# Performance work log

Measured on AMD Instinct MI355X. Metric: run time of the kernel, lower is better.

Reference implementation:

```python
import jax, jax.numpy as jnp
import numpy as np

N = 50000      # num nodes
E = 400000     # num edges
B = 64         # num graphs
D_IN = 768
DIMS = [512, 256, 128]
CH = 64        # classifier hidden
NC = 2         # num classes
EPS = 1e-5


def setup_inputs() -> dict:
    key = jax.random.key(0)
    ks = jax.random.split(key, 12)
    inp = {}
    inp["x"] = jax.random.normal(ks[0], (N, D_IN), jnp.float32)
    inp["edge_index"] = jax.random.randint(ks[1], (2, E), 0, N, dtype=jnp.int32)
    inp["batch"] = jnp.sort(jax.random.randint(ks[2], (N,), 0, B, dtype=jnp.int32))
    dims = [D_IN] + DIMS
    for i in range(3):
        inp[f"W{i}"] = jax.random.normal(ks[3 + i], (dims[i], dims[i + 1]), jnp.float32) / np.sqrt(dims[i]).astype(np.float32)
        inp[f"b{i}"] = jnp.zeros((dims[i + 1],), jnp.float32)
        inp[f"gamma{i}"] = jnp.ones((dims[i + 1],), jnp.float32)
        inp[f"beta{i}"] = jnp.zeros((dims[i + 1],), jnp.float32)
    inp["Wc1"] = jax.random.normal(ks[6], (2 * DIMS[-1], CH), jnp.float32) / np.sqrt(2 * DIMS[-1]).astype(np.float32)
    inp["bc1"] = jnp.zeros((CH,), jnp.float32)
    inp["gamma_c"] = jnp.ones((CH,), jnp.float32)
    inp["beta_c"] = jnp.zeros((CH,), jnp.float32)
    inp["Wc2"] = jax.random.normal(ks[7], (CH, NC), jnp.float32) / np.sqrt(CH).astype(np.float32)
    inp["bc2"] = jnp.zeros((NC,), jnp.float32)
    return inp


def _batchnorm(h, gamma, beta):
    # training-mode BatchNorm1d: biased batch statistics over the node axis
    m = jnp.mean(h, axis=0)
    v = jnp.var(h, axis=0)
    return (h - m) * jax.lax.rsqrt(v + EPS) * gamma + beta


def _forward(x, edge_index, batch, params):
    # GCN normalization with self-loops: norm_e = deg[src]^-1/2 * deg[dst]^-1/2
    loops = jnp.arange(N, dtype=edge_index.dtype)
    src = jnp.concatenate([edge_index[0], loops])
    dst = jnp.concatenate([edge_index[1], loops])
    deg = jax.ops.segment_sum(jnp.ones_like(dst, jnp.float32), dst, num_segments=N)
    dis = jax.lax.rsqrt(deg)  # deg >= 1 due to self loops
    norm = dis[src] * dis[dst]  # [E+N]

    n_layers = len(params)
    h = x
    for i, (W, b, g, be) in enumerate(params):
        hw = h @ W                                   # [N, out_dim]
        msg = hw[src] * norm[:, None]                # gather + scale, [E+N, out_dim]
        h = jax.ops.segment_sum(msg, dst, num_segments=N) + b
        h = _batchnorm(h, g, be)
        if i < n_layers - 1:
            h = jax.nn.relu(h)
        # dropout: identity in eval; residual never fires (dims 512/256 != 128)
    return h


def reference(x, edge_index, batch,
              W0, b0, gamma0, beta0,
              W1, b1, gamma1, beta1,
              W2, b2, gamma2, beta2,
              Wc1, bc1, gamma_c, beta_c, Wc2, bc2):
    params = [(W0, b0, gamma0, beta0), (W1, b1, gamma1, beta1), (W2, b2, gamma2, beta2)]
    h = _forward(x, edge_index, batch, params)       # [N, 128]

    # mean_max global pooling over graphs
    ones = jnp.ones((N,), jnp.float32)
    cnt = jnp.maximum(jax.ops.segment_sum(ones, batch, num_segments=B), 1.0)
    mean_pool = jax.ops.segment_sum(h, batch, num_segments=B) / cnt[:, None]
    max_pool = jax.ops.segment_max(h, batch, num_segments=B)
    g = jnp.concatenate([mean_pool, max_pool], axis=1)  # [B, 256]

    # classifier: Linear -> ReLU -> BatchNorm -> (Dropout=id) -> Linear
    hc = jax.nn.relu(g @ Wc1 + bc1)
    hc = _batchnorm(hc, gamma_c, beta_c)
    logits = hc @ Wc2 + bc2                          # [B, 2]
    return logits
```

## Files before the change

### kernel.cpp

```cpp
#include <hip/hip_runtime.h>
#include <cstddef>

#define NN 50000
#define EE 400000
#define BB 64
#define MP 50048
#define BN_EPS 1e-5f
#define PSEG 32

typedef __attribute__((ext_vector_type(8))) short s16x8;
typedef __attribute__((ext_vector_type(4))) float f32x4;
typedef __attribute__((ext_vector_type(8))) _Float16 f16x8;

#define GLOAD_LDS16(g, l) __builtin_amdgcn_global_load_lds( \
    (const __attribute__((address_space(1))) void*)(g),     \
    (__attribute__((address_space(3))) void*)(l), 16, 0, 0)

__global__ void fill_f32(float* __restrict__ p, int n, float v) {
    int i = blockIdx.x * blockDim.x + threadIdx.x;
    if (i < n) p[i] = v;
}

__global__ void fill_i32(int* __restrict__ p, int n, int v) {
    int i = blockIdx.x * blockDim.x + threadIdx.x;
    if (i < n) p[i] = v;
}

__global__ void deg_edges(const int* __restrict__ ei, int* __restrict__ deg) {
    int e = blockIdx.x * blockDim.x + threadIdx.x;
    if (e < EE) atomicAdd(&deg[ei[EE + e]], 1);
}

__global__ void cvt_wt_planes(const float* __restrict__ W,
                              unsigned short* __restrict__ Wh,
                              unsigned short* __restrict__ Wl,
                              int K, int N) {
    int i = blockIdx.x * blockDim.x + threadIdx.x;
    if (i >= K * N) return;
    int k = i / N, n = i % N;
    float f = W[i];
    unsigned int fb = __float_as_uint(f);
    unsigned int hif = fb & 0xFFFF0000u;
    float lo = f - __uint_as_float(hif);
    Wh[(size_t)n * K + k] = (unsigned short)(hif >> 16);
    Wl[(size_t)n * K + k] = (unsigned short)(__float_as_uint(lo) >> 16);
}

__global__ __launch_bounds__(256) void scan_block(const int* __restrict__ deg,
                                                  int* __restrict__ rowptr,
                                                  int* __restrict__ bsum,
                                                  float* __restrict__ dis) {
    __shared__ int tmp[256];
    int tid = threadIdx.x;
    int i = blockIdx.x * 256 + tid;
    int v = (i < NN) ? deg[i] : 0;
    if (i < NN) dis[i] = rsqrtf((float)v + 1.0f);
    tmp[tid] = v;
    __syncthreads();
#pragma unroll
    for (int off = 1; off < 256; off <<= 1) {
        int t = (tid >= off) ? tmp[tid - off] : 0;
        __syncthreads();
        tmp[tid] += t;
        __syncthreads();
    }
    if (i < NN) rowptr[i] = tmp[tid] - v;
    if (tid == 255) bsum[blockIdx.x] = tmp[255];
}

__global__ __launch_bounds__(256) void scan_sums(const int* __restrict__ bsum,
                                                 int* __restrict__ boff, int nb) {
    __shared__ int tmp[256];
    int tid = threadIdx.x;
    int v = (tid < nb) ? bsum[tid] : 0;
    tmp[tid] = v;
    __syncthreads();
#pragma unroll
    for (int off = 1; off < 256; off <<= 1) {
        int t = (tid >= off) ? tmp[tid - off] : 0;
        __syncthreads();
        tmp[tid] += t;
        __syncthreads();
    }
    boff[tid] = tmp[tid] - v;
}

__global__ void scan_fixup(int* __restrict__ rowptr, const int* __restrict__ boff,
                           int* __restrict__ cursor) {
    int i = blockIdx.x * blockDim.x + threadIdx.x;
    if (i < NN) {
        int v = rowptr[i] + boff[i >> 8];
        rowptr[i] = v;
        cursor[i] = v;
    }
    if (i == 0) rowptr[NN] = EE;
}

__global__ void fill_csr(const int* __restrict__ ei, int* __restrict__ cursor,
                         int* __restrict__ csr_src) {
    int e = blockIdx.x * blockDim.x + threadIdx.x;
    if (e >= EE) return;
    int s = ei[e];
    int t = ei[EE + e];
    int pos = atomicAdd(&cursor[t], 1);
    csr_src[pos] = s;
}

static __device__ __forceinline__ void unpack_pk(const uint4& u0, const uint4& u1,
                                                 s16x8& h, s16x8& l) {
    unsigned int p[8] = {u0.x, u0.y, u0.z, u0.w, u1.x, u1.y, u1.z, u1.w};
    union { s16x8 v; unsigned int u[4]; } H, L;
#pragma unroll
    for (int k = 0; k < 4; ++k) {
        H.u[k] = (p[2 * k + 1] & 0xFFFF0000u) | (p[2 * k] >> 16);
        L.u[k] = (p[2 * k + 1] << 16) | (p[2 * k] & 0xFFFFu);
    }
    h = H.v; l = L.v;
}

static __device__ __forceinline__ void unpack_f32(const uint4& u0, const uint4& u1,
                                                  s16x8& h, s16x8& l) {
    unsigned int e[8] = {u0.x, u0.y, u0.z, u0.w, u1.x, u1.y, u1.z, u1.w};
    unsigned int hi[8], lo[8];
#pragma unroll
    for (int j = 0; j < 8; ++j) {
        hi[j] = e[j] & 0xFFFF0000u;
        float lf = __uint_as_float(e[j]) - __uint_as_float(hi[j]);
        lo[j] = __float_as_uint(lf);
    }
    union { s16x8 v; unsigned int u[4]; } H, L;
#pragma unroll
    for (int k = 0; k < 4; ++k) {
        H.u[k] = (hi[2 * k + 1]) | (hi[2 * k] >> 16);
        L.u[k] = (lo[2 * k + 1] & 0xFFFF0000u) | (lo[2 * k] >> 16);
    }
    h = H.v; l = L.v;
}

template <int AMODE>
__global__ __launch_bounds__(256) void gemm_split3(const unsigned int* __restrict__ A,
                                                   const unsigned short* __restrict__ Bh,
                                                   const unsigned short* __restrict__ Bl,
                                                   _Float16* __restrict__ C,
                                                   const float* __restrict__ dis,
                                                   int K, int N) {
    __shared__ unsigned int As[128 * 32];
    __shared__ unsigned short Bsh[128 * 32];
    __shared__ unsigned short Bsl[128 * 32];
    const int tid = threadIdx.x;
    const int w  = tid >> 6;
    const int lw = tid & 63;
    const int lo = lw & 15;
    const int hi = lw >> 4;
    const int wr = w >> 1, wc = w & 1;
    const int rowBase = blockIdx.y * 128;
    const int colBase = blockIdx.x * 128;

    const int arow = w * 8 + (lw >> 3);
    const int acol = (lw & 7) * 4;
    const int brow = w * 16 + (lw >> 2);
    const int bcol = (lw & 3) * 8;

    f32x4 acc[4][4];
#pragma unroll
    for (int m = 0; m < 4; ++m)
#pragma unroll
        for (int n = 0; n < 4; ++n) acc[m][n] = (f32x4){0.f, 0.f, 0.f, 0.f};

    for (int k0 = 0; k0 < K; k0 += 32) {
#pragma unroll
        for (int i = 0; i < 4; ++i) {
            int gr = rowBase + i * 32 + arow;
            gr = (gr < NN) ? gr : (NN - 1);
            GLOAD_LDS16(A + (size_t)gr * K + k0 + acol, (char*)As + i * 4096 + w * 1024);
        }
#pragma unroll
        for (int j = 0; j < 2; ++j) {
            int gc = colBase + j * 64 + brow;
            GLOAD_LDS16(Bh + (size_t)gc * K + k0 + bcol, (char*)Bsh + j * 4096 + w * 1024);
            GLOAD_LDS16(Bl + (size_t)gc * K + k0 + bcol, (char*)Bsl + j * 4096 + w * 1024);
        }
        __syncthreads();

        s16x8 ah[4], al[4], bh[4], bl[4];
#pragma unroll
        for (int m = 0; m < 4; ++m) {
            int r = wr * 64 + m * 16 + lo;
            uint4 u0 = *(const uint4*)&As[r * 32 + hi * 8];
            uint4 u1 = *(const uint4*)&As[r * 32 + hi * 8 + 4];
            if (AMODE == 0) unpack_f32(u0, u1, ah[m], al[m]);
            else            unpack_pk(u0, u1, ah[m], al[m]);
        }
#pragma unroll
        for (int n = 0; n < 4; ++n) {
            int r = wc * 64 + n * 16 + lo;
            bh[n] = *(const s16x8*)&Bsh[r * 32 + hi * 8];
            bl[n] = *(const s16x8*)&Bsl[r * 32 + hi * 8];
        }
#pragma unroll
        for (int m = 0; m < 4; ++m)
#pragma unroll
            for (int n = 0; n < 4; ++n) {
                acc[m][n] = __builtin_amdgcn_mfma_f32_16x16x32_bf16(ah[m], bh[n], acc[m][n], 0, 0, 0);
                acc[m][n] = __builtin_amdgcn_mfma_f32_16x16x32_bf16(ah[m], bl[n], acc[m][n], 0, 0, 0);
                acc[m][n] = __builtin_amdgcn_mfma_f32_16x16x32_bf16(al[m], bh[n], acc[m][n], 0, 0, 0);
            }
        __syncthreads();
    }

#pragma unroll
    for (int m = 0; m < 4; ++m) {
        int row0 = rowBase + wr * 64 + m * 16 + hi * 4;
#pragma unroll
        for (int j = 0; j < 4; ++j) {
            int r = row0 + j;
            float ds = dis[(r < NN) ? r : (NN - 1)];
#pragma unroll
            for (int n = 0; n < 4; ++n) {
                int col = colBase + wc * 64 + n * 16 + lo;
                C[(size_t)r * N + col] = (_Float16)(ds * acc[m][n][j]);
            }
        }
    }
}

__global__ __launch_bounds__(256) void agg_gather(const _Float16* __restrict__ hws,
                                                  float* __restrict__ agg,
                                                  const int* __restrict__ rowptr,
                                                  const int* __restrict__ csr_src,
                                                  const float* __restrict__ dis,
                                                  const float* __restrict__ bias,
                                                  int D) {
    const int tpn = D >> 3;
    const int npb = 256 / tpn;
    const int local = threadIdx.x / tpn;
    const int lane = threadIdx.x % tpn;
    const int n = blockIdx.x * npb + local;
    if (n >= NN) return;
    const int dq = lane * 8;

    f16x8 sv = *(const f16x8*)&hws[(size_t)n * D + dq];
    float a[8];
#pragma unroll
    for (int j = 0; j < 8; ++j) a[j] = (float)sv[j];

    int e0 = rowptr[n], e1 = rowptr[n + 1];
    int e = e0;
    for (; e + 4 <= e1; e += 4) {
        int s0 = csr_src[e + 0];
        int s1 = csr_src[e + 1];
        int s2 = csr_src[e + 2];
        int s3 = csr_src[e + 3];
        f16x8 v0 = *(const f16x8*)&hws[(size_t)s0 * D + dq];
        f16x8 v1 = *(const f16x8*)&hws[(size_t)s1 * D + dq];
        f16x8 v2 = *(const f16x8*)&hws[(size_t)s2 * D + dq];
        f16x8 v3 = *(const f16x8*)&hws[(size_t)s3 * D + dq];
#pragma unroll
        for (int j = 0; j < 8; ++j)
            a[j] += ((float)v0[j] + (float)v1[j]) + ((float)v2[j] + (float)v3[j]);
    }
    for (; e < e1; ++e) {
        int s = csr_src[e];
        f16x8 v = *(const f16x8*)&hws[(size_t)s * D + dq];
#pragma unroll
        for (int j = 0; j < 8; ++j) a[j] += (float)v[j];
    }

    float din = dis[n];
    f32x4 o0, o1;
#pragma unroll
    for (int j = 0; j < 4; ++j) o0[j] = din * a[j] + bias[dq + j];
#pragma unroll
    for (int j = 0; j < 4; ++j) o1[j] = din * a[4 + j] + bias[dq + 4 + j];
    *(f32x4*)&agg[(size_t)n * D + dq] = o0;
    *(f32x4*)&agg[(size_t)n * D + dq + 4] = o1;
}

__global__ void bn_stats(const float* __restrict__ h, float* __restrict__ stats, int D) {
    int d = blockIdx.x * blockDim.x + threadIdx.x;
    if (d >= D) return;
    float s = 0.f, ss = 0.f;
    for (int n = blockIdx.y; n < NN; n += gridDim.y) {
        float v = h[(size_t)n * D + d];
        s += v;
        ss += v * v;
    }
    atomicAdd(&stats[d], s);
    atomicAdd(&stats[D + d], ss);
}

__global__ void bn_apply(unsigned int* __restrict__ buf,
                         const float* __restrict__ stats,
                         const float* __restrict__ gamma, const float* __restrict__ beta,
                         int D) {
    size_t i = (size_t)blockIdx.x * blockDim.x + threadIdx.x;
    if (i >= (size_t)NN * D) return;
    int d = (int)(i % (size_t)D);
    float mean = stats[d] * (1.0f / NN);
    float var  = stats[D + d] * (1.0f / NN) - mean * mean;
    float f = (__uint_as_float(buf[i]) - mean) * rsqrtf(var + BN_EPS) * gamma[d] + beta[d];
    f = fmaxf(f, 0.f);
    unsigned int fb = __float_as_uint(f);
    unsigned int hif = fb & 0xFFFF0000u;
    float lf = f - __uint_as_float(hif);
    buf[i] = hif | (__float_as_uint(lf) >> 16);
}

__global__ void bn_coef(const float* __restrict__ stats,
                        const float* __restrict__ gamma, const float* __restrict__ beta,
                        float* __restrict__ c1, float* __restrict__ c2, int D) {
    int d = blockIdx.x * blockDim.x + threadIdx.x;
    if (d >= D) return;
    float mean = stats[d] * (1.0f / NN);
    float var  = stats[D + d] * (1.0f / NN) - mean * mean;
    float r = rsqrtf(var + BN_EPS) * gamma[d];
    c1[d] = r;
    c2[d] = beta[d] - mean * r;
}

__global__ void find_starts(const int* __restrict__ batch, int* __restrict__ start) {
    int n = blockIdx.x * blockDim.x + threadIdx.x;
    if (n >= NN) return;
    int bc = batch[n];
    int bp = (n == 0) ? -1 : batch[n - 1];
    for (int g = bp + 1; g <= bc; ++g) start[g] = n;
    if (n == NN - 1) {
        for (int g = bc + 1; g <= BB; ++g) start[g] = NN;
    }
}

__global__ void pool_part(const float* __restrict__ h, const int* __restrict__ start,
                          const float* __restrict__ c1, const float* __restrict__ c2,
                          float* __restrict__ part) {
    int b = blockIdx.x;
    int seg = blockIdx.y;
    int d = threadIdx.x;
    int s0 = start[b], s1 = start[b + 1];
    int len = s1 - s0;
    int a = s0 + (int)((long long)len * seg / PSEG);
    int e = s0 + (int)((long long)len * (seg + 1) / PSEG);
    float a1 = c1[d], a2 = c2[d];
    float sum = 0.f;
    float mx = -3.402823466e+38f;
    for (int n = a; n < e; ++n) {
        float v = a1 * h[(size_t)n * 128 + d] + a2;
        sum += v;
        mx = fmaxf(mx, v);
    }
    part[(size_t)(b * PSEG + seg) * 256 + d] = sum;
    part[(size_t)(b * PSEG + seg) * 256 + 128 + d] = mx;
}

__global__ void pool_reduce(const float* __restrict__ part, const int* __restrict__ start,
                            float* __restrict__ pool) {
    int b = blockIdx.x;
    int d = threadIdx.x;
    float sum = 0.f;
    float mx = -3.402823466e+38f;
    for (int s = 0; s < PSEG; ++s) {
        sum += part[(size_t)(b * PSEG + s) * 256 + d];
        mx = fmaxf(mx, part[(size_t)(b * PSEG + s) * 256 + 128 + d]);
    }
    float cnt = fmaxf((float)(start[b + 1] - start[b]), 1.0f);
    pool[b * 256 + d] = sum / cnt;
    pool[b * 256 + 128 + d] = mx;
}

__global__ __launch_bounds__(256) void classifier_kernel(
        const float* __restrict__ pool,
        const float* __restrict__ Wc1, const float* __restrict__ bc1,
        const float* __restrict__ gc, const float* __restrict__ bec,
        const float* __restrict__ Wc2, const float* __restrict__ bc2,
        float* __restrict__ out) {
    __shared__ float hc[64][65];
    __shared__ float cmean[64];
    __shared__ float crstd[64];
    int tid = threadIdx.x;

    for (int i = tid; i < 64 * 64; i += 256) {
        int r = i / 64, c = i % 64;
        float acc = bc1[c];
        for (int k = 0; k < 256; ++k)
            acc += pool[r * 256 + k] * Wc1[k * 64 + c];
        hc[r][c] = fmaxf(acc, 0.f);
    }
    __syncthreads();

    if (tid < 64) {
        float s = 0.f, ss = 0.f;
        for (int r = 0; r < 64; ++r) {
            float v = hc[r][tid];
            s += v;
            ss += v * v;
        }
        float m = s * (1.0f / 64.0f);
        float var = ss * (1.0f / 64.0f) - m * m;
        cmean[tid] = m;
        crstd[tid] = rsqrtf(var + BN_EPS);
    }
    __syncthreads();

    if (tid < 128) {
        int r = tid / 2, k = tid % 2;
        float acc = bc2[k];
        for (int c = 0; c < 64; ++c) {
            float v = (hc[r][c] - cmean[c]) * crstd[c] * gc[c] + bec[c];
            acc += v * Wc2[c * 2 + k];
        }
        out[r * 2 + k] = acc;
    }
}

extern "C" void kernel_launch(void* const* d_in, const int* in_sizes, int n_in,
                              void* d_out, int out_size, void* d_ws, size_t ws_size,
                              hipStream_t stream) {
    const float* x     = (const float*)d_in[0];
    const int*   ei    = (const int*)d_in[1];
    const int*   batch = (const int*)d_in[2];
    const float* W[3]  = {(const float*)d_in[3], (const float*)d_in[7], (const float*)d_in[11]};
    const float* bbv[3] = {(const float*)d_in[4], (const float*)d_in[8], (const float*)d_in[12]};
    const float* gm[3] = {(const float*)d_in[5], (const float*)d_in[9], (const float*)d_in[13]};
    const float* bt[3] = {(const float*)d_in[6], (const float*)d_in[10], (const float*)d_in[14]};
    const float* Wc1 = (const float*)d_in[15];
    const float* bc1 = (const float*)d_in[16];
    const float* gc  = (const float*)d_in[17];
    const float* bec = (const float*)d_in[18];
    const float* Wc2 = (const float*)d_in[19];
    const float* bc2 = (const float*)d_in[20];
    float* out = (float*)d_out;

    char* p = (char*)d_ws;
    _Float16* hw = (_Float16*)p; p += (size_t)MP * 512 * 2;
    unsigned int* agg = (unsigned int*)p; p += (size_t)NN * 512 * 4;
    unsigned short* Wh[3];
    unsigned short* Wl[3];
    Wh[0] = (unsigned short*)p; p += (size_t)512 * 768 * 2;
    Wl[0] = (unsigned short*)p; p += (size_t)512 * 768 * 2;
    Wh[1] = (unsigned short*)p; p += (size_t)256 * 512 * 2;
    Wl[1] = (unsigned short*)p; p += (size_t)256 * 512 * 2;
    Wh[2] = (unsigned short*)p; p += (size_t)128 * 256 * 2;
    Wl[2] = (unsigned short*)p; p += (size_t)128 * 256 * 2;
    float* dis   = (float*)p; p += (size_t)NN * 4;
    float* stats = (float*)p; p += 1024 * 4;
    float* pool  = (float*)p; p += (size_t)BB * 256 * 4;
    float* part  = (float*)p; p += (size_t)BB * PSEG * 256 * 4;
    int* deg_i   = (int*)p; p += (size_t)NN * 4;
    int* rowptr  = (int*)p; p += (size_t)(NN + 1) * 4;
    int* cursor  = (int*)p; p += (size_t)NN * 4;
    int* bsum    = (int*)p; p += 256 * 4;
    int* boff    = (int*)p; p += 256 * 4;
    int* csr_src = (int*)p; p += (size_t)EE * 4;
    int* start   = (int*)p; p += (BB + 1) * 4;
    float* c1 = stats + 512;
    float* c2 = stats + 640;

    const int nb = (NN + 255) / 256;

    cvt_wt_planes<<<(768 * 512 + 255) / 256, 256, 0, stream>>>(W[0], Wh[0], Wl[0], 768, 512);
    cvt_wt_planes<<<(512 * 256 + 255) / 256, 256, 0, stream>>>(W[1], Wh[1], Wl[1], 512, 256);
    cvt_wt_planes<<<(256 * 128 + 255) / 256, 256, 0, stream>>>(W[2], Wh[2], Wl[2], 256, 128);

    fill_i32<<<nb, 256, 0, stream>>>(deg_i, NN, 0);
    deg_edges<<<(EE + 255) / 256, 256, 0, stream>>>(ei, deg_i);
    scan_block<<<nb, 256, 0, stream>>>(deg_i, rowptr, bsum, dis);
    scan_sums<<<1, 256, 0, stream>>>(bsum, boff, nb);
    scan_fixup<<<nb, 256, 0, stream>>>(rowptr, boff, cursor);
    fill_csr<<<(EE + 255) / 256, 256, 0, stream>>>(ei, cursor, csr_src);

    const int dims[4] = {768, 512, 256, 128};

    for (int l = 0; l < 3; ++l) {
        int K = dims[l], D = dims[l + 1];

        dim3 gg(D / 128, MP / 128);
        if (l == 0)
            gemm_split3<0><<<gg, 256, 0, stream>>>((const unsigned int*)x, Wh[0], Wl[0],
                                                   hw, dis, K, D);
        else
            gemm_split3<1><<<gg, 256, 0, stream>>>(agg, Wh[l], Wl[l], hw, dis, K, D);

        int tpn = D / 8;
        int npb = 256 / tpn;
        agg_gather<<<(NN + npb - 1) / npb, 256, 0, stream>>>(hw, (float*)agg, rowptr, csr_src,
                                                             dis, bbv[l], D);

        fill_f32<<<(2 * D + 255) / 256, 256, 0, stream>>>(stats, 2 * D, 0.0f);
        bn_stats<<<dim3((D + 255) / 256, 256), 256, 0, stream>>>((const float*)agg, stats, D);
        if (l < 2) {
            size_t tot = (size_t)NN * D;
            bn_apply<<<(int)((tot + 255) / 256), 256, 0, stream>>>(agg, stats, gm[l], bt[l], D);
        } else {
            bn_coef<<<1, 128, 0, stream>>>(stats, gm[2], bt[2], c1, c2, 128);
        }
    }

    find_starts<<<nb, 256, 0, stream>>>(batch, start);
    dim3 pg(BB, PSEG);
    pool_part<<<pg, 128, 0, stream>>>((const float*)agg, start, c1, c2, part);
    pool_reduce<<<BB, 128, 0, stream>>>(part, start, pool);
    classifier_kernel<<<1, 256, 0, stream>>>(pool, Wc1, bc1, gc, bec, Wc2, bc2, out);
}
```

Measured before the change: 820.0 us.

## Double-buffer LDS tiles in split-bf16 GEMM to overlap loads with MFMA

The GEMM now keeps two LDS buffers for the A and B tiles and issues the global-to-LDS loads for the next K-step before computing on the current one. Each iteration ends with a vmcnt wait and a barrier instead of a load-sync-compute-sync sequence. The goal is to hide global memory latency behind the three-way MFMA work. It doubles LDS use to 64KB per block, which may lower occupancy.

New measurement: 808.0 us. Within noise of the previous version (-1.5%).

```diff
diff --git a/kernel.cpp b/kernel.cpp
--- a/kernel.cpp
+++ b/kernel.cpp
@@ -144,9 +144,9 @@
                                                    _Float16* __restrict__ C,
                                                    const float* __restrict__ dis,
                                                    int K, int N) {
-    __shared__ unsigned int As[128 * 32];
-    __shared__ unsigned short Bsh[128 * 32];
-    __shared__ unsigned short Bsl[128 * 32];
+    __shared__ unsigned int As[2][128 * 32];
+    __shared__ unsigned short Bsh[2][128 * 32];
+    __shared__ unsigned short Bsl[2][128 * 32];
     const int tid = threadIdx.x;
     const int w  = tid >> 6;
     const int lw = tid & 63;
@@ -167,35 +167,47 @@
 #pragma unroll
         for (int n = 0; n < 4; ++n) acc[m][n] = (f32x4){0.f, 0.f, 0.f, 0.f};
 
-    for (int k0 = 0; k0 < K; k0 += 32) {
-#pragma unroll
-        for (int i = 0; i < 4; ++i) {
-            int gr = rowBase + i * 32 + arow;
-            gr = (gr < NN) ? gr : (NN - 1);
-            GLOAD_LDS16(A + (size_t)gr * K + k0 + acol, (char*)As + i * 4096 + w * 1024);
-        }
-#pragma unroll
-        for (int j = 0; j < 2; ++j) {
-            int gc = colBase + j * 64 + brow;
-            GLOAD_LDS16(Bh + (size_t)gc * K + k0 + bcol, (char*)Bsh + j * 4096 + w * 1024);
-            GLOAD_LDS16(Bl + (size_t)gc * K + k0 + bcol, (char*)Bsl + j * 4096 + w * 1024);
-        }
-        __syncthreads();
+#define STAGE(buf, k0s) do {                                                        \
+    _Pragma("unroll")                                                               \
+    for (int i_ = 0; i_ < 4; ++i_) {                                                \
+        int gr_ = rowBase + i_ * 32 + arow;                                         \
+        gr_ = (gr_ < NN) ? gr_ : (NN - 1);                                          \
+        GLOAD_LDS16(A + (size_t)gr_ * K + (k0s) + acol,                             \
+                    (char*)&As[buf][0] + i_ * 4096 + w * 1024);                     \
+    }                                                                               \
+    _Pragma("unroll")                                                               \
+    for (int j_ = 0; j_ < 2; ++j_) {                                                \
+        int gc_ = colBase + j_ * 64 + brow;                                         \
+        GLOAD_LDS16(Bh + (size_t)gc_ * K + (k0s) + bcol,                            \
+                    (char*)&Bsh[buf][0] + j_ * 4096 + w * 1024);                    \
+        GLOAD_LDS16(Bl + (size_t)gc_ * K + (k0s) + bcol,                            \
+                    (char*)&Bsl[buf][0] + j_ * 4096 + w * 1024);                    \
+    }                                                                               \
+} while (0)
+
+    STAGE(0, 0);
+    asm volatile("s_waitcnt vmcnt(0)" ::: "memory");
+    __builtin_amdgcn_s_barrier();
+
+    const int nt = K >> 5;
+    int cur = 0;
+    for (int t = 0; t < nt; ++t) {
+        if (t + 1 < nt) STAGE(cur ^ 1, (t + 1) << 5);
 
         s16x8 ah[4], al[4], bh[4], bl[4];
 #pragma unroll
         for (int m = 0; m < 4; ++m) {
             int r = wr * 64 + m * 16 + lo;
-            uint4 u0 = *(const uint4*)&As[r * 32 + hi * 8];
-            uint4 u1 = *(const uint4*)&As[r * 32 + hi * 8 + 4];
+            uint4 u0 = *(const uint4*)&As[cur][r * 32 + hi * 8];
+            uint4 u1 = *(const uint4*)&As[cur][r * 32 + hi * 8 + 4];
             if (AMODE == 0) unpack_f32(u0, u1, ah[m], al[m]);
             else            unpack_pk(u0, u1, ah[m], al[m]);
         }
 #pragma unroll
         for (int n = 0; n < 4; ++n) {
             int r = wc * 64 + n * 16 + lo;
-            bh[n] = *(const s16x8*)&Bsh[r * 32 + hi * 8];
-            bl[n] = *(const s16x8*)&Bsl[r * 32 + hi * 8];
+            bh[n] = *(const s16x8*)&Bsh[cur][r * 32 + hi * 8];
+            bl[n] = *(const s16x8*)&Bsl[cur][r * 32 + hi * 8];
         }
 #pragma unroll
         for (int m = 0; m < 4; ++m)
@@ -205,8 +217,12 @@
                 acc[m][n] = __builtin_amdgcn_mfma_f32_16x16x32_bf16(ah[m], bl[n], acc[m][n], 0, 0, 0);
                 acc[m][n] = __builtin_amdgcn_mfma_f32_16x16x32_bf16(al[m], bh[n], acc[m][n], 0, 0, 0);
             }
-        __syncthreads();
-    }
+
+        asm volatile("s_waitcnt vmcnt(0)" ::: "memory");
+        __builtin_amdgcn_s_barrier();
+        cur ^= 1;
+    }
+#undef STAGE
 
 #pragma unroll
     for (int m = 0; m < 4; ++m) {
```
